# Optimization experiments

Hardware: AMD Instinct MI355X
Metric: run time of the kernel (lower is better)

The kernel has to match this reference:

```python
import jax, jax.numpy as jnp
import numpy as np

DIM = 4096
N_HEADS = 32
N_KV_HEADS = 8
HEAD_DIM = DIM // N_HEADS  # 128
SEQLEN = 2048
BATCH = 2
ROPE_THETA = 10000.0


def _precompute_freqs(seqlen, head_dim, theta):
    # matches torchtitan precompute_freqs_cis: freqs over even indices
    freqs = 1.0 / (theta ** (np.arange(0, head_dim, 2)[: head_dim // 2].astype(np.float32) / head_dim))
    t = np.arange(seqlen, dtype=np.float32)
    ang = np.outer(t, freqs)  # (S, head_dim//2)
    return jnp.asarray(np.cos(ang)), jnp.asarray(np.sin(ang))


def setup_inputs() -> dict:
    key = jax.random.key(0)
    kx, kq, kk, kv, ko = jax.random.split(key, 5)
    x = jax.random.normal(kx, (BATCH, SEQLEN, DIM), dtype=jnp.float32)
    wq = jax.random.normal(kq, (N_HEADS * HEAD_DIM, DIM), dtype=jnp.float32) * 0.02
    wk = jax.random.normal(kk, (N_KV_HEADS * HEAD_DIM, DIM), dtype=jnp.float32) * 0.02
    wv = jax.random.normal(kv, (N_KV_HEADS * HEAD_DIM, DIM), dtype=jnp.float32) * 0.02
    wo = jax.random.normal(ko, (DIM, N_HEADS * HEAD_DIM), dtype=jnp.float32) * 0.02
    cos, sin = _precompute_freqs(SEQLEN, HEAD_DIM, ROPE_THETA)
    return {"x": x, "cos": cos, "sin": sin, "wq": wq, "wk": wk, "wv": wv, "wo": wo}


def _apply_rope(t, cos, sin):
    # t: (B, S, H, hd); pairs (t[...,2i], t[...,2i+1]) rotated by angle
    tr = t.reshape(*t.shape[:-1], -1, 2)
    a, b = tr[..., 0], tr[..., 1]
    c = cos[None, :, None, :]  # (1, S, 1, hd//2)
    s = sin[None, :, None, :]
    out = jnp.stack([a * c - b * s, a * s + b * c], axis=-1)
    return out.reshape(t.shape)


def reference(x, cos, sin, wq, wk, wv, wo):
    B, S, D = x.shape
    hd = 2 * cos.shape[-1]
    H = wq.shape[0] // hd
    KVH = wk.shape[0] // hd
    n_rep = H // KVH

    q = (x @ wq.T).reshape(B, S, H, hd)
    k = (x @ wk.T).reshape(B, S, KVH, hd)
    v = (x @ wv.T).reshape(B, S, KVH, hd)

    q = _apply_rope(q, cos, sin)
    k = _apply_rope(k, cos, sin)

    # GQA: repeat_interleave kv heads (kept implicit via reshape of q into groups)
    qg = q.reshape(B, S, KVH, n_rep, hd)
    scale = 1.0 / jnp.sqrt(jnp.asarray(hd, dtype=x.dtype))
    # scores: (B, KVH, n_rep, S_q, S_k)
    scores = jnp.einsum("bsgrd,btgd->bgrst", qg, k) * scale
    causal = jnp.tril(jnp.ones((S, S), dtype=bool))
    scores = jnp.where(causal[None, None, None], scores, jnp.asarray(-1e30, dtype=scores.dtype))
    probs = jax.nn.softmax(scores, axis=-1)
    out = jnp.einsum("bgrst,btgd->bsgrd", probs, v).reshape(B, S, H * hd)
    return out @ wo.T
```

## Files before the change

kernel.cpp:

```cpp
#include <hip/hip_runtime.h>
#include <hip/hip_bf16.h>
#include <stdint.h>

#define DIM    4096
#define NH     32
#define NKVH   8
#define HD     128
#define SEQ    2048
#define BATCH  2
#define MTOT   (BATCH*SEQ)
#define SCALE  0.08838834764831845f

typedef __bf16 bf16_t;
typedef __bf16 bf16x8 __attribute__((ext_vector_type(8)));
typedef float  f32x4  __attribute__((ext_vector_type(4)));

#define AS1 __attribute__((address_space(1)))
#define AS3 __attribute__((address_space(3)))

__device__ __forceinline__ void gload_lds16(const void* g, void* l) {
    __builtin_amdgcn_global_load_lds((const AS1 void*)g, (AS3 void*)l, 16, 0, 0);
}

__device__ __forceinline__ void fence_barrier() {
    asm volatile("" ::: "memory");
    __builtin_amdgcn_s_barrier();
    asm volatile("" ::: "memory");
}

__global__ __launch_bounds__(256)
void cvt_f32_bf16(const float* __restrict__ in, bf16_t* __restrict__ out, int n4) {
    for (int i = blockIdx.x * blockDim.x + threadIdx.x; i < n4;
         i += gridDim.x * blockDim.x) {
        float4 v = reinterpret_cast<const float4*>(in)[i];
        union { bf16_t b[4]; uint2 u; } t;
        t.b[0] = (bf16_t)v.x; t.b[1] = (bf16_t)v.y;
        t.b[2] = (bf16_t)v.z; t.b[3] = (bf16_t)v.w;
        reinterpret_cast<uint2*>(out)[i] = t.u;
    }
}


__device__ __forceinline__ void stage_half(const bf16_t* gbase, int kt, int h,
                                           bf16_t* ldsdst, int tid, int w) {
#pragma unroll
    for (int t2 = 0; t2 < 2; ++t2) {
        int s = t2 * 512 + tid;
        int r = s >> 3, c = s & 7;
        gload_lds16(gbase + (size_t)(h * 128 + r) * DIM + kt + ((c ^ (r & 7)) * 8),
                    ldsdst + (size_t)(t2 * 512 + w * 64) * 8);
    }
}

__device__ __forceinline__ void read_a8(bf16x8* a, const bf16_t* Ahalf,
                                        int kk, int lr, int lg) {
#pragma unroll
    for (int mi = 0; mi < 8; ++mi) {
        int r = mi * 16 + lr;
        a[mi] = *(const bf16x8*)(Ahalf + r * 64 + ((kk * 4 + lg) ^ (r & 7)) * 8);
    }
}

__device__ __forceinline__ void read_b4(bf16x8* b, const bf16_t* Bhalf,
                                        int kk, int rb, int lg) {
#pragma unroll
    for (int ni = 0; ni < 4; ++ni) {
        int r = rb + ni * 16;
        b[ni] = *(const bf16x8*)(Bhalf + r * 64 + ((kk * 4 + lg) ^ (r & 7)) * 8);
    }
}

template<int MODE>
__global__ __launch_bounds__(512, 2)
void gemm8(const bf16_t* __restrict__ A,
           const bf16_t* __restrict__ B0,
           const bf16_t* __restrict__ B1,
           float* __restrict__ outF,
           bf16_t* __restrict__ outQ,
           bf16_t* __restrict__ outV,
           const float* __restrict__ cosT,
           const float* __restrict__ sinT) {
    __shared__ __align__(16) bf16_t As[2][2][128 * 64];
    __shared__ __align__(16) bf16_t Bs[2][2][128 * 64];

    const int tid = threadIdx.x;
    const int l = tid & 63;
    const int w = tid >> 6;
    const int wm = w >> 2, wn = w & 3;
    const int lr = l & 15, lg = l >> 4;
    const int rb = (wn & 1) * 64 + lr;

    const int rowBase = blockIdx.x * 256;
    const int ct = blockIdx.y;

    const bf16_t* Ap = A + (size_t)rowBase * DIM;
    const bf16_t* Bp;
    if (MODE == 2) Bp = (ct < 4) ? (B0 + (size_t)ct * 256 * DIM)
                                 : (B1 + (size_t)(ct - 4) * 256 * DIM);
    else           Bp = B0 + (size_t)ct * 256 * DIM;

    f32x4 acc[8][4] = {};
    bf16x8 a0[8], a1[8], b0[4], b1[4];

    stage_half(Bp, 0,  0, &Bs[0][0][0], tid, w);
    stage_half(Bp, 0,  1, &Bs[0][1][0], tid, w);
    stage_half(Ap, 0,  0, &As[0][0][0], tid, w);
    stage_half(Ap, 0,  1, &As[0][1][0], tid, w);
    stage_half(Bp, 64, 0, &Bs[1][0][0], tid, w);
    stage_half(Bp, 64, 1, &Bs[1][1][0], tid, w);
    asm volatile("s_waitcnt vmcnt(4)" ::: "memory");
    fence_barrier();

    const int NT = DIM / 64;
    for (int j = 0; j < NT; ++j) {
        const int buf = j & 1;
        const int ktA = (j + 1 < NT ? j + 1 : NT - 1) * 64;
        const int ktB = (j + 2 < NT ? j + 2 : NT - 1) * 64;
        const bf16_t* Ahalf = &As[buf][wm][0];
        const bf16_t* Bhalf = &Bs[buf][wn >> 1][0];

        read_a8(a0, Ahalf, 0, lr, lg);
        read_b4(b0, Bhalf, 0, rb, lg);
        stage_half(Ap, ktA, 0, &As[buf ^ 1][0][0], tid, w);
        fence_barrier();
        __builtin_amdgcn_s_setprio(1);
#pragma unroll
        for (int mi = 0; mi < 8; ++mi) {
            acc[mi][0] = __builtin_amdgcn_mfma_f32_16x16x32_bf16(a0[mi], b0[0], acc[mi][0], 0, 0, 0);
            acc[mi][1] = __builtin_amdgcn_mfma_f32_16x16x32_bf16(a0[mi], b0[1], acc[mi][1], 0, 0, 0);
        }
        __builtin_amdgcn_s_setprio(0);
        __builtin_amdgcn_sched_barrier(0);
        fence_barrier();

        read_b4(b1, Bhalf, 1, rb, lg);
        stage_half(Ap, ktA, 1, &As[buf ^ 1][1][0], tid, w);
        fence_barrier();
        __builtin_amdgcn_s_setprio(1);
#pragma unroll
        for (int mi = 0; mi < 8; ++mi) {
            acc[mi][2] = __builtin_amdgcn_mfma_f32_16x16x32_bf16(a0[mi], b0[2], acc[mi][2], 0, 0, 0);
            acc[mi][3] = __builtin_amdgcn_mfma_f32_16x16x32_bf16(a0[mi], b0[3], acc[mi][3], 0, 0, 0);
        }
        __builtin_amdgcn_s_setprio(0);
        __builtin_amdgcn_sched_barrier(0);
        asm volatile("s_waitcnt lgkmcnt(0)" ::: "memory");
        fence_barrier();

        read_a8(a1, Ahalf, 1, lr, lg);
        stage_half(Bp, ktB, 0, &Bs[buf][0][0], tid, w);
        fence_barrier();
        __builtin_amdgcn_s_setprio(1);
#pragma unroll
        for (int mi = 0; mi < 8; ++mi) {
            acc[mi][0] = __builtin_amdgcn_mfma_f32_16x16x32_bf16(a1[mi], b1[0], acc[mi][0], 0, 0, 0);
            acc[mi][1] = __builtin_amdgcn_mfma_f32_16x16x32_bf16(a1[mi], b1[1], acc[mi][1], 0, 0, 0);
        }
        __builtin_amdgcn_s_setprio(0);
        __builtin_amdgcn_sched_barrier(0);
        fence_barrier();

        stage_half(Bp, ktB, 1, &Bs[buf][1][0], tid, w);
        fence_barrier();
        __builtin_amdgcn_s_setprio(1);
#pragma unroll
        for (int mi = 0; mi < 8; ++mi) {
            acc[mi][2] = __builtin_amdgcn_mfma_f32_16x16x32_bf16(a1[mi], b1[2], acc[mi][2], 0, 0, 0);
            acc[mi][3] = __builtin_amdgcn_mfma_f32_16x16x32_bf16(a1[mi], b1[3], acc[mi][3], 0, 0, 0);
        }
        __builtin_amdgcn_s_setprio(0);
        __builtin_amdgcn_sched_barrier(0);
        asm volatile("s_waitcnt vmcnt(4)" ::: "memory");
        fence_barrier();
    }

#pragma unroll
    for (int mi = 0; mi < 8; ++mi) {
        int gmBase = rowBase + wm * 128 + mi * 16 + lg * 4;
#pragma unroll
        for (int ni = 0; ni < 4; ++ni) {
            f32x4 v4 = acc[mi][ni];
            int gn = ct * 256 + wn * 64 + ni * 16 + lr;
            if (MODE == 0) {
#pragma unroll
                for (int i = 0; i < 4; ++i)
                    outF[(size_t)(gmBase + i) * DIM + gn] = v4[i];
            } else if (MODE == 1) {
                int h = gn >> 7, d = gn & 127, pi2 = d >> 1;
#pragma unroll
                for (int i = 0; i < 4; ++i) {
                    float v = v4[i];
                    float pvv = __shfl_xor(v, 1);
                    int gm = gmBase + i;
                    int bb = gm >> 11, sidx = gm & (SEQ - 1);
                    float c = cosT[sidx * 64 + pi2], sn = sinT[sidx * 64 + pi2];
                    float o = (d & 1) ? (pvv * sn + v * c) : (v * c - pvv * sn);
                    outQ[((size_t)(bb * NH + h) * SEQ + sidx) * HD + d] = (bf16_t)o;
                }
            } else {
                if (ct < 4) {
                    int h = gn >> 7, d = gn & 127, pi2 = d >> 1;
#pragma unroll
                    for (int i = 0; i < 4; ++i) {
                        float v = v4[i];
                        float pvv = __shfl_xor(v, 1);
                        int gm = gmBase + i;
                        int bb = gm >> 11, sidx = gm & (SEQ - 1);
                        float c = cosT[sidx * 64 + pi2], sn = sinT[sidx * 64 + pi2];
                        float o = (d & 1) ? (pvv * sn + v * c) : (v * c - pvv * sn);
                        outQ[((size_t)(bb * NKVH + h) * SEQ + sidx) * HD + d] = (bf16_t)o;
                    }
                } else {
                    int gnv = (ct - 4) * 256 + wn * 64 + ni * 16 + lr;
                    int kvh = gnv >> 7, d = gnv & 127;
#pragma unroll
                    for (int i = 0; i < 4; ++i) {
                        float dummy = __shfl_xor(v4[i], 1); (void)dummy;
                        int gm = gmBase + i;
                        int bb = gm >> 11, sidx = gm & (SEQ - 1);
                        outV[((size_t)(bb * NKVH + kvh) * HD + d) * SEQ + sidx] = (bf16_t)v4[i];
                    }
                }
            }
        }
    }
}

__global__ __launch_bounds__(256, 2)
void attn_fwd(const bf16_t* __restrict__ Qr,
              const bf16_t* __restrict__ Kr,
              const bf16_t* __restrict__ Vt,
              bf16_t* __restrict__ Ob) {
    __shared__ __align__(16) bf16_t Ks[2][64 * 128];
    __shared__ __align__(16) bf16_t Vs[2][128 * 64];
    __shared__ __align__(16) bf16_t Ps[4][32 * 64];

    const int tid = threadIdx.x;
    const int l  = tid & 63;
    const int w  = tid >> 6;
    const int lr = l & 15, lg = l >> 4;
    const int e  = lr & 7;

    const int qt  = 15 - (blockIdx.x >> 6);
    const int bh  = blockIdx.x & 63;
    const int b   = bh >> 5;
    const int h   = bh & 31;
    const int kvh = h >> 2;
    const int q0  = qt * 128;
    const int nt  = 2 * qt + 2;
    const int qmin = q0 + w * 32;

    const bf16_t* kbase = Kr + (size_t)(b * NKVH + kvh) * SEQ * HD;
    const bf16_t* vbase = Vt + (size_t)(b * NKVH + kvh) * HD * SEQ;

    bf16x8 qf[2][4];
    const bf16_t* qp = Qr + ((size_t)(b * NH + h) * SEQ + qmin + lr) * HD;
#pragma unroll
    for (int mi = 0; mi < 2; ++mi)
#pragma unroll
        for (int kk = 0; kk < 4; ++kk)
            qf[mi][kk] = *(const bf16x8*)(qp + (size_t)mi * 16 * HD + kk * 32 + lg * 8);

    f32x4 oacc[2][8] = {};
    float mrow[2] = {-1e30f, -1e30f};
    float lsum[2] = {0.f, 0.f};

#pragma unroll
    for (int t2 = 0; t2 < 4; ++t2) {
        int s = t2 * 256 + tid;
        { int r = s >> 4, g = (s & 15) ^ (r & 7);
          gload_lds16(kbase + (size_t)r * HD + g * 8,
                      &Ks[0][(size_t)(t2 * 256 + w * 64) * 8]); }
        { int r = s >> 3, g = (s & 7) ^ (r & 7);
          gload_lds16(vbase + (size_t)r * SEQ + g * 8,
                      &Vs[0][(size_t)(t2 * 256 + w * 64) * 8]); }
    }
    __syncthreads();

    int cur = 0;
    for (int t = 0; t < nt; ++t) {
        if (t + 1 < nt) {
            const int kv1 = (t + 1) * 64;
#pragma unroll
            for (int t2 = 0; t2 < 4; ++t2) {
                int s = t2 * 256 + tid;
                { int r = s >> 4, g = (s & 15) ^ (r & 7);
                  gload_lds16(kbase + (size_t)(kv1 + r) * HD + g * 8,
                              &Ks[cur ^ 1][(size_t)(t2 * 256 + w * 64) * 8]); }
                { int r = s >> 3, g = (s & 7) ^ (r & 7);
                  gload_lds16(vbase + (size_t)r * SEQ + kv1 + g * 8,
                              &Vs[cur ^ 1][(size_t)(t2 * 256 + w * 64) * 8]); }
            }
        }

        const bool active = (t * 64) <= (qmin + 31);
        if (active) {
            const bool needMask = (t * 64 + 63) > qmin;

            f32x4 sf[2][4] = {};
#pragma unroll
            for (int kk = 0; kk < 4; ++kk)
#pragma unroll
                for (int nf = 0; nf < 4; ++nf) {
                    bf16x8 kf = *(const bf16x8*)(
                        &Ks[cur][(nf * 16 + lr) * 128 + ((kk * 4 + lg) ^ e) * 8]);
#pragma unroll
                    for (int mi = 0; mi < 2; ++mi)
                        sf[mi][nf] = __builtin_amdgcn_mfma_f32_16x16x32_bf16(
                            kf, qf[mi][kk], sf[mi][nf], 0, 0, 0);
                }

            float aO[2][4];
#pragma unroll
            for (int mi = 0; mi < 2; ++mi) {
                const int qrow = qmin + mi * 16 + lr;
                float mt = -1e30f;
#pragma unroll
                for (int nf = 0; nf < 4; ++nf)
#pragma unroll
                    for (int i = 0; i < 4; ++i) {
                        float sc = sf[mi][nf][i] * SCALE;
                        if (needMask && (t * 64 + nf * 16 + lg * 4 + i) > qrow)
                            sc = -1e30f;
                        sf[mi][nf][i] = sc;
                        mt = fmaxf(mt, sc);
                    }
                mt = fmaxf(mt, __shfl_xor(mt, 16));
                mt = fmaxf(mt, __shfl_xor(mt, 32));
                float mnew = fmaxf(mrow[mi], mt);
                float alpha = __expf(mrow[mi] - mnew);
                mrow[mi] = mnew;
                float rs = 0.f;
#pragma unroll
                for (int nf = 0; nf < 4; ++nf)
#pragma unroll
                    for (int i = 0; i < 4; ++i) {
                        float p = __expf(sf[mi][nf][i] - mnew);
                        sf[mi][nf][i] = p;
                        rs += p;
                    }
                rs += __shfl_xor(rs, 16);
                rs += __shfl_xor(rs, 32);
                lsum[mi] = lsum[mi] * alpha + rs;
#pragma unroll
                for (int i = 0; i < 4; ++i)
                    aO[mi][i] = __shfl(alpha, lg * 4 + i);
            }

#pragma unroll
            for (int mi = 0; mi < 2; ++mi)
#pragma unroll
                for (int df = 0; df < 8; ++df)
#pragma unroll
                    for (int i = 0; i < 4; ++i)
                        oacc[mi][df][i] *= aO[mi][i];

#pragma unroll
            for (int mi = 0; mi < 2; ++mi)
#pragma unroll
                for (int nf = 0; nf < 4; ++nf) {
                    union { bf16_t bb[4]; uint2 u; } pk;
#pragma unroll
                    for (int i = 0; i < 4; ++i) pk.bb[i] = (bf16_t)sf[mi][nf][i];
                    int addr = (mi * 16 + lr) * 64 +
                               (((nf * 2 + (lg >> 1)) ^ e) << 3) + (lg & 1) * 4;
                    *(uint2*)(&Ps[w][addr]) = pk.u;
                }
            asm volatile("s_waitcnt lgkmcnt(0)" ::: "memory");
            __builtin_amdgcn_sched_barrier(0);

            bf16x8 pf[2][2];
#pragma unroll
            for (int mi = 0; mi < 2; ++mi)
#pragma unroll
                for (int k2 = 0; k2 < 2; ++k2)
                    pf[mi][k2] = *(const bf16x8*)(
                        &Ps[w][(mi * 16 + lr) * 64 + ((k2 * 4 + lg) ^ e) * 8]);
#pragma unroll
            for (int df = 0; df < 8; ++df)
#pragma unroll
                for (int k2 = 0; k2 < 2; ++k2) {
                    bf16x8 vf = *(const bf16x8*)(
                        &Vs[cur][(df * 16 + lr) * 64 + ((k2 * 4 + lg) ^ e) * 8]);
#pragma unroll
                    for (int mi = 0; mi < 2; ++mi)
                        oacc[mi][df] = __builtin_amdgcn_mfma_f32_16x16x32_bf16(
                            pf[mi][k2], vf, oacc[mi][df], 0, 0, 0);
                }
        }
        __syncthreads();
        cur ^= 1;
    }

#pragma unroll
    for (int mi = 0; mi < 2; ++mi) {
        float ls[4];
#pragma unroll
        for (int i = 0; i < 4; ++i)
            ls[i] = 1.f / __shfl(lsum[mi], lg * 4 + i);
#pragma unroll
        for (int df = 0; df < 8; ++df)
#pragma unroll
            for (int i = 0; i < 4; ++i) {
                float o = oacc[mi][df][i] * ls[i];
                int gm = b * SEQ + qmin + mi * 16 + lg * 4 + i;
                int gn = h * HD + df * 16 + lr;
                Ob[(size_t)gm * DIM + gn] = (bf16_t)o;
            }
    }
}

extern "C" void kernel_launch(void* const* d_in, const int* in_sizes, int n_in,
                              void* d_out, int out_size, void* d_ws, size_t ws_size,
                              hipStream_t stream) {
    const float* x    = (const float*)d_in[0];
    const float* cosT = (const float*)d_in[1];
    const float* sinT = (const float*)d_in[2];
    const float* wq   = (const float*)d_in[3];
    const float* wk   = (const float*)d_in[4];
    const float* wv   = (const float*)d_in[5];
    const float* wo   = (const float*)d_in[6];

    bf16_t* p = (bf16_t*)d_ws;
    bf16_t* xb  = p; p += (size_t)MTOT * DIM;
    bf16_t* wqb = p; p += (size_t)DIM * DIM;
    bf16_t* wkb = p; p += (size_t)NKVH * HD * DIM;
    bf16_t* wvb = p; p += (size_t)NKVH * HD * DIM;
    bf16_t* wob = p; p += (size_t)DIM * DIM;
    bf16_t* Qr  = p; p += (size_t)MTOT * DIM;
    bf16_t* Kr  = p; p += (size_t)BATCH * NKVH * SEQ * HD;
    bf16_t* Vt  = p; p += (size_t)BATCH * NKVH * HD * SEQ;
    bf16_t* Ob  = p; p += (size_t)MTOT * DIM;

    cvt_f32_bf16<<<1024, 256, 0, stream>>>(x,  xb,  MTOT * DIM / 4);
    cvt_f32_bf16<<<1024, 256, 0, stream>>>(wq, wqb, DIM * DIM / 4);
    cvt_f32_bf16<<<512,  256, 0, stream>>>(wk, wkb, NKVH * HD * DIM / 4);
    cvt_f32_bf16<<<512,  256, 0, stream>>>(wv, wvb, NKVH * HD * DIM / 4);
    cvt_f32_bf16<<<1024, 256, 0, stream>>>(wo, wob, DIM * DIM / 4);

    gemm8<1><<<dim3(16, 16), 512, 0, stream>>>(
        xb, wqb, nullptr, nullptr, Qr, nullptr, cosT, sinT);
    gemm8<2><<<dim3(16, 8), 512, 0, stream>>>(
        xb, wkb, wvb, nullptr, Kr, Vt, cosT, sinT);

    attn_fwd<<<1024, 256, 0, stream>>>(Qr, Kr, Vt, Ob);

    gemm8<0><<<dim3(16, 16), 512, 0, stream>>>(
        Ob, wob, nullptr, (float*)d_out, nullptr, nullptr, nullptr, nullptr);
}
```

Baseline: 593.3 us.

## Restructure GEMM main loop into two-stage prefetch and merge weight conversions

The GEMM main loop drops its four barrier-separated sub-phases per K tile. It now loads the whole next-but-one A and B tile at once, keeps two tiles in flight (vmcnt 8), and prefetches the next tile's first-half fragments from LDS before the loop iteration ends. This cuts barriers per iteration from six to two and overlaps LDS reads with MFMA. The four weight conversion launches become one kernel with a larger grid, which relies on the bf16 weight buffers sitting contiguously in the workspace. The new buffering changes which LDS buffer is overwritten when, so correctness depends on the barrier and waitcnt placement being sufficient.

```diff
diff --git a/kernel.cpp b/kernel.cpp
--- a/kernel.cpp
+++ b/kernel.cpp
@@ -33,6 +33,31 @@
     for (int i = blockIdx.x * blockDim.x + threadIdx.x; i < n4;
          i += gridDim.x * blockDim.x) {
         float4 v = reinterpret_cast<const float4*>(in)[i];
+        union { bf16_t b[4]; uint2 u; } t;
+        t.b[0] = (bf16_t)v.x; t.b[1] = (bf16_t)v.y;
+        t.b[2] = (bf16_t)v.z; t.b[3] = (bf16_t)v.w;
+        reinterpret_cast<uint2*>(out)[i] = t.u;
+    }
+}
+
+__global__ __launch_bounds__(256)
+void cvt_weights(const float* __restrict__ wq, const float* __restrict__ wk,
+                 const float* __restrict__ wv, const float* __restrict__ wo,
+                 bf16_t* __restrict__ out) {
+    const int n0 = DIM * DIM / 4;
+    const int n1 = NKVH * HD * DIM / 4;
+    const int n2 = NKVH * HD * DIM / 4;
+    const int n3 = DIM * DIM / 4;
+    const int ntot = n0 + n1 + n2 + n3;
+    for (int i = blockIdx.x * blockDim.x + threadIdx.x; i < ntot;
+         i += gridDim.x * blockDim.x) {
+        const float* src;
+        int k = i;
+        if (k < n0) src = wq;
+        else if ((k -= n0) < n1) src = wk;
+        else if ((k -= n1) < n2) src = wv;
+        else { k -= n2; src = wo; }
+        float4 v = reinterpret_cast<const float4*>(src)[k];
         union { bf16_t b[4]; uint2 u; } t;
         t.b[0] = (bf16_t)v.x; t.b[1] = (bf16_t)v.y;
         t.b[2] = (bf16_t)v.z; t.b[3] = (bf16_t)v.w;
@@ -89,6 +114,7 @@
     const int wm = w >> 2, wn = w & 3;
     const int lr = l & 15, lg = l >> 4;
     const int rb = (wn & 1) * 64 + lr;
+    const int bh2 = wn >> 1;
 
     const int rowBase = blockIdx.x * 256;
     const int ct = blockIdx.y;
@@ -102,76 +128,63 @@
     f32x4 acc[8][4] = {};
     bf16x8 a0[8], a1[8], b0[4], b1[4];
 
+    const int NT = DIM / 64;
+
+    stage_half(Ap, 0,  0, &As[0][0][0], tid, w);
+    stage_half(Ap, 0,  1, &As[0][1][0], tid, w);
     stage_half(Bp, 0,  0, &Bs[0][0][0], tid, w);
     stage_half(Bp, 0,  1, &Bs[0][1][0], tid, w);
-    stage_half(Ap, 0,  0, &As[0][0][0], tid, w);
-    stage_half(Ap, 0,  1, &As[0][1][0], tid, w);
+    stage_half(Ap, 64, 0, &As[1][0][0], tid, w);
+    stage_half(Ap, 64, 1, &As[1][1][0], tid, w);
     stage_half(Bp, 64, 0, &Bs[1][0][0], tid, w);
     stage_half(Bp, 64, 1, &Bs[1][1][0], tid, w);
-    asm volatile("s_waitcnt vmcnt(4)" ::: "memory");
+    asm volatile("s_waitcnt vmcnt(8)" ::: "memory");
     fence_barrier();
-
-    const int NT = DIM / 64;
+    read_a8(a0, &As[0][wm][0], 0, lr, lg);
+    read_b4(b0, &Bs[0][bh2][0], 0, rb, lg);
+
     for (int j = 0; j < NT; ++j) {
         const int buf = j & 1;
-        const int ktA = (j + 1 < NT ? j + 1 : NT - 1) * 64;
-        const int ktB = (j + 2 < NT ? j + 2 : NT - 1) * 64;
-        const bf16_t* Ahalf = &As[buf][wm][0];
-        const bf16_t* Bhalf = &Bs[buf][wn >> 1][0];
-
-        read_a8(a0, Ahalf, 0, lr, lg);
-        read_b4(b0, Bhalf, 0, rb, lg);
-        stage_half(Ap, ktA, 0, &As[buf ^ 1][0][0], tid, w);
-        fence_barrier();
+
+        read_a8(a1, &As[buf][wm][0], 1, lr, lg);
+        read_b4(b1, &Bs[buf][bh2][0], 1, rb, lg);
         __builtin_amdgcn_s_setprio(1);
 #pragma unroll
         for (int mi = 0; mi < 8; ++mi) {
             acc[mi][0] = __builtin_amdgcn_mfma_f32_16x16x32_bf16(a0[mi], b0[0], acc[mi][0], 0, 0, 0);
             acc[mi][1] = __builtin_amdgcn_mfma_f32_16x16x32_bf16(a0[mi], b0[1], acc[mi][1], 0, 0, 0);
-        }
-        __builtin_amdgcn_s_setprio(0);
-        __builtin_amdgcn_sched_barrier(0);
-        fence_barrier();
-
-        read_b4(b1, Bhalf, 1, rb, lg);
-        stage_half(Ap, ktA, 1, &As[buf ^ 1][1][0], tid, w);
-        fence_barrier();
-        __builtin_amdgcn_s_setprio(1);
-#pragma unroll
-        for (int mi = 0; mi < 8; ++mi) {
             acc[mi][2] = __builtin_amdgcn_mfma_f32_16x16x32_bf16(a0[mi], b0[2], acc[mi][2], 0, 0, 0);
             acc[mi][3] = __builtin_amdgcn_mfma_f32_16x16x32_bf16(a0[mi], b0[3], acc[mi][3], 0, 0, 0);
         }
         __builtin_amdgcn_s_setprio(0);
-        __builtin_amdgcn_sched_barrier(0);
         asm volatile("s_waitcnt lgkmcnt(0)" ::: "memory");
         fence_barrier();
 
-        read_a8(a1, Ahalf, 1, lr, lg);
-        stage_half(Bp, ktB, 0, &Bs[buf][0][0], tid, w);
-        fence_barrier();
+        {
+            const int t2i = (j + 2 < NT) ? (j + 2) : (NT - 1);
+            const int kt2 = t2i * 64;
+            bf16_t* Adst0 = &As[t2i & 1][0][0];
+            bf16_t* Bdst0 = &Bs[t2i & 1][0][0];
+            stage_half(Ap, kt2, 0, Adst0, tid, w);
+            stage_half(Ap, kt2, 1, Adst0 + 128 * 64, tid, w);
+            stage_half(Bp, kt2, 0, Bdst0, tid, w);
+            stage_half(Bp, kt2, 1, Bdst0 + 128 * 64, tid, w);
+        }
         __builtin_amdgcn_s_setprio(1);
 #pragma unroll
         for (int mi = 0; mi < 8; ++mi) {
             acc[mi][0] = __builtin_amdgcn_mfma_f32_16x16x32_bf16(a1[mi], b1[0], acc[mi][0], 0, 0, 0);
             acc[mi][1] = __builtin_amdgcn_mfma_f32_16x16x32_bf16(a1[mi], b1[1], acc[mi][1], 0, 0, 0);
-        }
-        __builtin_amdgcn_s_setprio(0);
-        __builtin_amdgcn_sched_barrier(0);
-        fence_barrier();
-
-        stage_half(Bp, ktB, 1, &Bs[buf][1][0], tid, w);
-        fence_barrier();
-        __builtin_amdgcn_s_setprio(1);
-#pragma unroll
-        for (int mi = 0; mi < 8; ++mi) {
             acc[mi][2] = __builtin_amdgcn_mfma_f32_16x16x32_bf16(a1[mi], b1[2], acc[mi][2], 0, 0, 0);
             acc[mi][3] = __builtin_amdgcn_mfma_f32_16x16x32_bf16(a1[mi], b1[3], acc[mi][3], 0, 0, 0);
         }
         __builtin_amdgcn_s_setprio(0);
-        __builtin_amdgcn_sched_barrier(0);
-        asm volatile("s_waitcnt vmcnt(4)" ::: "memory");
+        asm volatile("s_waitcnt vmcnt(8)" ::: "memory");
         fence_barrier();
+        if (j + 1 < NT) {
+            read_a8(a0, &As[buf ^ 1][wm][0], 0, lr, lg);
+            read_b4(b0, &Bs[buf ^ 1][bh2][0], 0, rb, lg);
+        }
     }
 
 #pragma unroll
@@ -432,11 +445,8 @@
     bf16_t* Vt  = p; p += (size_t)BATCH * NKVH * HD * SEQ;
     bf16_t* Ob  = p; p += (size_t)MTOT * DIM;
 
-    cvt_f32_bf16<<<1024, 256, 0, stream>>>(x,  xb,  MTOT * DIM / 4);
-    cvt_f32_bf16<<<1024, 256, 0, stream>>>(wq, wqb, DIM * DIM / 4);
-    cvt_f32_bf16<<<512,  256, 0, stream>>>(wk, wkb, NKVH * HD * DIM / 4);
-    cvt_f32_bf16<<<512,  256, 0, stream>>>(wv, wvb, NKVH * HD * DIM / 4);
-    cvt_f32_bf16<<<1024, 256, 0, stream>>>(wo, wob, DIM * DIM / 4);
+    cvt_f32_bf16<<<2048, 256, 0, stream>>>(x, xb, MTOT * DIM / 4);
+    cvt_weights<<<2048, 256, 0, stream>>>(wq, wk, wv, wo, wqb);
 
     gemm8<1><<<dim3(16, 16), 512, 0, stream>>>(
         xb, wqb, nullptr, nullptr, Qr, nullptr, cosT, sinT);
```

Result: faster. 520.1 us (-12.3%).
